# Optimization experiments

Measured on AMD Instinct MI355X. Metric: run time of the kernel, lower is better.

## Reference

```python
import jax, jax.numpy as jnp
import numpy as np

N = 20000; E = 320000; IN = 512; H = 4; C = 128; HC = H * C; SD = 2; SE = 128
NEG = 0.01      # nn.LeakyReLU default slope (post-norm activations)
ATT_NEG = 0.2   # GATv2 attention LeakyReLU slope


def _gatv2(x, wl, bl, wr, br, att, bias, src, dst, concat):
    # PyG GATv2Conv (eval mode, add_self_loops already applied to src/dst)
    n = x.shape[0]
    xl = (x @ wl.T + bl).reshape(n, H, C)   # source-side projection
    xr = (x @ wr.T + br).reshape(n, H, C)   # target-side projection
    e = jax.nn.leaky_relu(xl[src] + xr[dst], ATT_NEG)        # [Etot, H, C]
    logits = jnp.einsum('ehc,hc->eh', e, att)                # [Etot, H]
    m = jax.ops.segment_max(logits, dst, num_segments=n)     # segment softmax over dst
    ez = jnp.exp(logits - m[dst])
    denom = jax.ops.segment_sum(ez, dst, num_segments=n)
    alpha = ez / denom[dst]
    out = jax.ops.segment_sum(xl[src] * alpha[:, :, None], dst, num_segments=n)  # [n, H, C]
    out = out.reshape(n, HC) if concat else out.mean(axis=1)
    return out + bias, alpha


def _bn(x, g, b):
    # BatchNorm1d, training-mode batch statistics (biased variance), eps=1e-5
    mu = x.mean(0)
    v = x.var(0)
    return g * (x - mu) * jax.lax.rsqrt(v + 1e-5) + b


def setup_inputs() -> dict:
    key = jax.random.key(0)
    ks = jax.random.split(key, 20)
    p = lambda i, shape: jax.random.normal(ks[i], shape, jnp.float32) * 0.05
    return dict(
        x=jax.random.normal(ks[0], (N, IN), jnp.float32),
        edge_index=jax.random.randint(ks[1], (2, E), 0, N),
        spatial_coords=jax.random.uniform(ks[2], (N, SD), dtype=jnp.float32),
        w1_l=p(3, (HC, IN)), b1_l=jnp.zeros((HC,)), w1_r=p(4, (HC, IN)), b1_r=jnp.zeros((HC,)),
        att1=p(5, (H, C)), bias1=jnp.zeros((HC,)), bn1_g=jnp.ones((HC,)), bn1_b=jnp.zeros((HC,)),
        w2_l=p(6, (HC, HC)), b2_l=jnp.zeros((HC,)), w2_r=p(7, (HC, HC)), b2_r=jnp.zeros((HC,)),
        att2=p(8, (H, C)), bias2=jnp.zeros((HC,)), bn2_g=jnp.ones((HC,)), bn2_b=jnp.zeros((HC,)),
        w3_l=p(9, (HC, HC)), b3_l=jnp.zeros((HC,)), w3_r=p(10, (HC, HC)), b3_r=jnp.zeros((HC,)),
        att3=p(11, (H, C)), bias3=jnp.zeros((C,)), bn3_g=jnp.ones((C,)), bn3_b=jnp.zeros((C,)),
        sp_w1=p(12, (SE, SD)), sp_b1=jnp.zeros((SE,)),
        sp_w2=p(13, (C, SE)), sp_b2=jnp.zeros((C,)),
        mha_in_w=p(14, (3 * SE, SE)), mha_in_b=jnp.zeros((3 * SE,)),
        mha_out_w=p(15, (SE, SE)), mha_out_b=jnp.zeros((SE,)),
        gate_w=p(16, (1, 2 * C)), gate_b=jnp.zeros((1,)),
    )


def reference(x, edge_index, spatial_coords,
              w1_l, b1_l, w1_r, b1_r, att1, bias1, bn1_g, bn1_b,
              w2_l, b2_l, w2_r, b2_r, att2, bias2, bn2_g, bn2_b,
              w3_l, b3_l, w3_r, b3_r, att3, bias3, bn3_g, bn3_b,
              sp_w1, sp_b1, sp_w2, sp_b2,
              mha_in_w, mha_in_b, mha_out_w, mha_out_b,
              gate_w, gate_b):
    loop = jnp.arange(N)
    src = jnp.concatenate([edge_index[0], loop])  # add self loops (PyG default)
    dst = jnp.concatenate([edge_index[1], loop])

    h1, a1 = _gatv2(x, w1_l, b1_l, w1_r, b1_r, att1, bias1, src, dst, True)
    h1 = jax.nn.leaky_relu(_bn(h1, bn1_g, bn1_b), NEG)
    h2, a2 = _gatv2(h1, w2_l, b2_l, w2_r, b2_r, att2, bias2, src, dst, True)
    h2 = jax.nn.leaky_relu(_bn(h2, bn2_g, bn2_b), NEG)
    z, a3 = _gatv2(h2, w3_l, b3_l, w3_r, b3_r, att3, bias3, src, dst, False)
    z = jax.nn.leaky_relu(_bn(z, bn3_g, bn3_b), NEG)

    # spatial embedding MLP (Linear -> LeakyReLU -> Linear -> LeakyReLU)
    emb = jax.nn.leaky_relu(spatial_coords @ sp_w1.T + sp_b1, NEG)
    emb = jax.nn.leaky_relu(emb @ sp_w2.T + sp_b2, NEG)
    # MultiheadAttention over a length-1 sequence: softmax over a single key is 1,
    # so output = W_o (W_v e + b_v) + b_o
    wv = mha_in_w[2 * SE:]
    bv = mha_in_b[2 * SE:]
    sp = (emb @ wv.T + bv) @ mha_out_w.T + mha_out_b  # [N, C]

    gate = jax.nn.softmax(jnp.concatenate([z, sp], axis=-1) @ gate_w.T + gate_b, axis=-1)  # [N,1] (all ones: size-1 softmax, faithful to source)
    z = gate * z + (1.0 - gate) * sp
    return z, a1, a2, a3, gate
```

## Files before the change

kernel.cpp:

```cpp
#include <hip/hip_runtime.h>
#include <math.h>

#define NN 20000
#define EE 320000
#define ETOT 340000
#define DEGCAP 128

typedef __attribute__((ext_vector_type(8))) short short8;
typedef __attribute__((ext_vector_type(4))) float f32x4;

__device__ __forceinline__ float lrelu(float x, float s) { return fmaxf(x, s * x); }
__device__ __forceinline__ float bf2f(ushort u) {
    union { uint i; float f; } c;
    c.i = ((uint)u) << 16;
    return c.f;
}
__device__ __forceinline__ ushort f2bf(float f) {
    uint u = __float_as_uint(f);
    uint r = (u + 0x7FFFu + ((u >> 16) & 1u)) >> 16;
    return (ushort)r;
}
__device__ __forceinline__ void gload16(const ushort* g, const ushort* l) {
    __builtin_amdgcn_global_load_lds((const __attribute__((address_space(1))) void*)g,
                                     (__attribute__((address_space(3))) void*)l, 16, 0, 0);
}

__global__ __launch_bounds__(1024) void k_scan(const int* __restrict__ counts, int* __restrict__ rstart) {
    __shared__ int sm[1024];
    int t = threadIdx.x;
    const int CH = 20;
    int base = t * CH;
    int loc[CH];
    int s = 0;
#pragma unroll
    for (int j = 0; j < CH; ++j) {
        int idx = base + j;
        int v = (idx < NN) ? counts[idx] : 0;
        loc[j] = s;
        s += v;
    }
    sm[t] = s;
    __syncthreads();
    for (int o = 1; o < 1024; o <<= 1) {
        int v = (t >= o) ? sm[t - o] : 0;
        __syncthreads();
        if (t >= o) sm[t] += v;
        __syncthreads();
    }
    int off = sm[t] - s;
#pragma unroll
    for (int j = 0; j < CH; ++j) {
        int idx = base + j;
        if (idx < NN) rstart[idx] = off + loc[j];
    }
    if (t == 1023) rstart[NN] = sm[1023];
}

__global__ void k_scatter(const int* __restrict__ ei, const int* __restrict__ rstart,
                          int* __restrict__ cursor, int* __restrict__ csr) {
    int i = blockIdx.x * blockDim.x + threadIdx.x;
    if (i >= ETOT) return;
    int d = (i < EE) ? ei[EE + i] : (i - EE);
    int pos = atomicAdd(&cursor[d], 1);
    csr[rstart[d] + pos] = i;
}

__global__ void k_prep(const float* __restrict__ x, const float* __restrict__ w0, const float* __restrict__ w1,
                       const float* __restrict__ w2, const float* __restrict__ w3, const float* __restrict__ w4,
                       const float* __restrict__ w5, ushort* __restrict__ xout, ushort* __restrict__ wout,
                       const int* __restrict__ ei, int* __restrict__ counts) {
    int b = blockIdx.x, t = threadIdx.x;
    if (b < 10000) {
        int i = (b * 256 + t) * 4;
        float4 v = *(const float4*)(x + i);
        uint2 pk;
        pk.x = (uint)f2bf(v.x) | ((uint)f2bf(v.y) << 16);
        pk.y = (uint)f2bf(v.z) | ((uint)f2bf(v.w) << 16);
        *(uint2*)(xout + i) = pk;
    } else if (b < 11536) {
        int q = (b - 10000) * 256 + t;
        if (q >= 6 * 65536) return;
        int which = q >> 16;
        int off = (q & 65535) << 2;
        const float* src = which == 0 ? w0 : which == 1 ? w1 : which == 2 ? w2 : which == 3 ? w3 : which == 4 ? w4 : w5;
        float4 v = *(const float4*)(src + off);
        uint2 pk;
        pk.x = (uint)f2bf(v.x) | ((uint)f2bf(v.y) << 16);
        pk.y = (uint)f2bf(v.z) | ((uint)f2bf(v.w) << 16);
        *(uint2*)(wout + which * 262144 + off) = pk;
    } else {
        int i = (b - 11536) * 256 + t;
        if (i >= ETOT) return;
        int d = (i < EE) ? ei[EE + i] : (i - EE);
        atomicAdd(&counts[d], 1);
    }
}

__global__ __launch_bounds__(512, 4) void k_gemm2(const ushort* __restrict__ A, const ushort* __restrict__ W,
                                                  const float* __restrict__ bl, const float* __restrict__ br,
                                                  ushort* __restrict__ XL, ushort* __restrict__ XR) {
    __shared__ ushort As[4][128][8];
    __shared__ ushort Bs[4][128][8];
    int tid = threadIdx.x;
    int wid = tid >> 6, lane = tid & 63;
    int wm = wid >> 2, wn = wid & 3;
    int bid = blockIdx.x;
    int L = (bid & 7) * 157 + (bid >> 3);
    int mt = L >> 3, nt = L & 7;
    int bm = mt * 128, bn = nt * 128;
    const float* bias = (nt >= 4) ? br : bl;
    ushort* C = (nt >= 4) ? XR : XL;
    int cb = bn - ((nt >= 4) ? 512 : 0);
    int lrow = lane & 15, lslot = lane >> 4;
    int r = tid & 127, ks = tid >> 7;
    int ar = bm + r;
    if (ar >= NN) ar = NN - 1;
    const ushort* gA = A + (size_t)ar * 512 + ks * 8;
    const ushort* gB = W + (size_t)(bn + r) * 512 + ks * 8;
    const ushort* lA = &As[0][0][0] + (size_t)(wid * 64) * 8;
    const ushort* lB = &Bs[0][0][0] + (size_t)(wid * 64) * 8;
    f32x4 acc[4][2] = {};
    for (int k0 = 0; k0 < 512; k0 += 32) {
        gload16(gA + k0, lA);
        gload16(gB + k0, lB);
        __syncthreads();
        short8 af[4], bfr[2];
#pragma unroll
        for (int i = 0; i < 4; ++i) af[i] = *(const short8*)&As[lslot][wm * 64 + i * 16 + lrow][0];
#pragma unroll
        for (int j = 0; j < 2; ++j) bfr[j] = *(const short8*)&Bs[lslot][wn * 32 + j * 16 + lrow][0];
#pragma unroll
        for (int i = 0; i < 4; ++i)
#pragma unroll
            for (int j = 0; j < 2; ++j)
                acc[i][j] = __builtin_amdgcn_mfma_f32_16x16x32_bf16(af[i], bfr[j], acc[i][j], 0, 0, 0);
        __syncthreads();
    }
#pragma unroll
    for (int i = 0; i < 4; ++i) {
#pragma unroll
        for (int j = 0; j < 2; ++j) {
            int gcol = cb + wn * 32 + j * 16 + lrow;
            float bv = bias[gcol];
            int growb = bm + wm * 64 + i * 16 + lslot * 4;
#pragma unroll
            for (int reg = 0; reg < 4; ++reg) {
                int grow = growb + reg;
                if (grow < NN) C[(size_t)grow * 512 + gcol] = f2bf(acc[i][j][reg] + bv);
            }
        }
    }
}

__global__ __launch_bounds__(256) void k_fused(const ushort* __restrict__ xl, const ushort* __restrict__ xr,
                                               const float* __restrict__ att, const int* __restrict__ ei,
                                               const int* __restrict__ rstart, const int* __restrict__ csr,
                                               const float* __restrict__ bias, float* __restrict__ alpha,
                                               ushort* __restrict__ dest, float* __restrict__ bzero, int meanHeads) {
    __shared__ float slg[4][DEGCAP][4];
    __shared__ int ssrc[4][DEGCAP];
    if (blockIdx.x == 0) {
        float4 z = {0.f, 0.f, 0.f, 0.f};
        ((float4*)bzero)[threadIdx.x] = z;
    }
    int w = threadIdx.x >> 6, lane = threadIdx.x & 63;
    int node = blockIdx.x * 4 + w;
    int s0 = rstart[node];
    int deg = rstart[node + 1] - s0;
    int hh = lane >> 4;
    short8 xrv = *(const short8*)(xr + (size_t)node * 512 + lane * 8);
    const float4* at = (const float4*)att + lane * 2;
    float4 a0 = at[0], a1 = at[1];
    float attv[8] = {a0.x, a0.y, a0.z, a0.w, a1.x, a1.y, a1.z, a1.w};
    float xrf[8];
#pragma unroll
    for (int j = 0; j < 8; ++j) xrf[j] = bf2f((ushort)xrv[j]);
    for (int i = lane; i < deg; i += 64) {
        int e = csr[s0 + i];
        ssrc[w][i < DEGCAP ? i : 0] = (e < EE) ? ei[e] : e - EE;
    }
    float m = -1e30f, denom = 0.f;
    float acc[8] = {};
    int scur = ssrc[w][0];
    short8 row = *(const short8*)(xl + (size_t)scur * 512 + lane * 8);
    for (int i = 0; i < deg; ++i) {
        short8 rown = row;
        if (i + 1 < deg) {
            int sn = ssrc[w][(i + 1) < DEGCAP ? (i + 1) : 0];
            rown = *(const short8*)(xl + (size_t)sn * 512 + lane * 8);
        }
        float rf[8];
#pragma unroll
        for (int j = 0; j < 8; ++j) rf[j] = bf2f((ushort)row[j]);
        float p = 0.f;
#pragma unroll
        for (int j = 0; j < 8; ++j) {
            float e = rf[j] + xrf[j];
            p = fmaf(fmaxf(e, 0.2f * e), attv[j], p);
        }
        p += __shfl_xor(p, 1);
        p += __shfl_xor(p, 2);
        p += __shfl_xor(p, 4);
        p += __shfl_xor(p, 8);
        if ((lane & 15) == 0 && i < DEGCAP) slg[w][i][hh] = p;
        if (p <= m) {
            float wg = __expf(p - m);
            denom += wg;
#pragma unroll
            for (int j = 0; j < 8; ++j) acc[j] = fmaf(wg, rf[j], acc[j]);
        } else {
            float sc = __expf(m - p);
            denom = fmaf(denom, sc, 1.f);
#pragma unroll
            for (int j = 0; j < 8; ++j) acc[j] = fmaf(acc[j], sc, rf[j]);
            m = p;
        }
        row = rown;
    }
    float rd = 1.f / denom;
    float m0 = __shfl(m, 0), m1 = __shfl(m, 16), m2 = __shfl(m, 32), m3 = __shfl(m, 48);
    float r0 = __shfl(rd, 0), r1 = __shfl(rd, 16), r2 = __shfl(rd, 32), r3 = __shfl(rd, 48);
    int nal = deg < DEGCAP ? deg : DEGCAP;
    for (int i = lane; i < nal; i += 64) {
        int e = csr[s0 + i];
        float4 l = *(const float4*)&slg[w][i][0];
        float4 av;
        av.x = __expf(l.x - m0) * r0;
        av.y = __expf(l.y - m1) * r1;
        av.z = __expf(l.z - m2) * r2;
        av.w = __expf(l.w - m3) * r3;
        *(float4*)(alpha + (size_t)e * 4) = av;
    }
#pragma unroll
    for (int j = 0; j < 8; ++j) acc[j] *= rd;
    if (!meanHeads) {
        int c = lane * 8;
        short8 o;
#pragma unroll
        for (int j = 0; j < 8; ++j) o[j] = (short)f2bf(acc[j] + bias[c + j]);
        *(short8*)(dest + (size_t)node * 512 + c) = o;
    } else {
#pragma unroll
        for (int j = 0; j < 8; ++j) {
            acc[j] += __shfl_xor(acc[j], 16);
            acc[j] += __shfl_xor(acc[j], 32);
        }
        if (lane < 16) {
            int c = lane * 8;
            short8 o;
#pragma unroll
            for (int j = 0; j < 8; ++j) o[j] = (short)f2bf(0.25f * acc[j] + bias[c + j]);
            *(short8*)(dest + (size_t)node * 128 + c) = o;
        }
    }
}

__global__ void k_bnstats(const ushort* __restrict__ X, float* __restrict__ s, float* __restrict__ s2, int npairs) {
    int t = threadIdx.x;
    if (t >= npairs) return;
    float a0 = 0.f, a1 = 0.f, q0 = 0.f, q1 = 0.f;
    for (int r = blockIdx.x; r < NN; r += gridDim.x) {
        uint p = ((const uint*)X)[r * npairs + t];
        float v0 = bf2f((ushort)(p & 0xffffu));
        float v1 = bf2f((ushort)(p >> 16));
        a0 += v0; q0 += v0 * v0;
        a1 += v1; q1 += v1 * v1;
    }
    atomicAdd(&s[2 * t], a0);
    atomicAdd(&s[2 * t + 1], a1);
    atomicAdd(&s2[2 * t], q0);
    atomicAdd(&s2[2 * t + 1], q1);
}

__global__ void k_bnapply(const ushort* __restrict__ X, const float* __restrict__ g, const float* __restrict__ b,
                          const float* __restrict__ bsum, const float* __restrict__ bsq, float* __restrict__ Yf,
                          ushort* __restrict__ Yb, float* __restrict__ gout, int mask4, int n4) {
    int i = blockIdx.x * blockDim.x + threadIdx.x;
    if (gout && i < NN) gout[i] = 1.0f;
    if (i >= n4) return;
    int c = (i & mask4) << 2;
    uint2 p = ((const uint2*)X)[i];
    float x0 = bf2f((ushort)(p.x & 0xffffu)), x1 = bf2f((ushort)(p.x >> 16));
    float x2 = bf2f((ushort)(p.y & 0xffffu)), x3 = bf2f((ushort)(p.y >> 16));
    float4 S = *(const float4*)(bsum + c);
    float4 Q = *(const float4*)(bsq + c);
    float4 G = *(const float4*)(g + c);
    float4 B = *(const float4*)(b + c);
    const float inv = 1.f / NN;
    float mx = S.x * inv, my = S.y * inv, mz = S.z * inv, mw = S.w * inv;
    float rx = rsqrtf(Q.x * inv - mx * mx + 1e-5f);
    float ry = rsqrtf(Q.y * inv - my * my + 1e-5f);
    float rz = rsqrtf(Q.z * inv - mz * mz + 1e-5f);
    float rw = rsqrtf(Q.w * inv - mw * mw + 1e-5f);
    float4 y;
    y.x = lrelu(G.x * (x0 - mx) * rx + B.x, 0.01f);
    y.y = lrelu(G.y * (x1 - my) * ry + B.y, 0.01f);
    y.z = lrelu(G.z * (x2 - mz) * rz + B.z, 0.01f);
    y.w = lrelu(G.w * (x3 - mw) * rw + B.w, 0.01f);
    if (Yb) {
        uint2 pk;
        pk.x = (uint)f2bf(y.x) | ((uint)f2bf(y.y) << 16);
        pk.y = (uint)f2bf(y.z) | ((uint)f2bf(y.w) << 16);
        *(uint2*)(Yb + (size_t)i * 4) = pk;
    } else {
        ((float4*)Yf)[i] = y;
    }
}

extern "C" void kernel_launch(void* const* d_in, const int* in_sizes, int n_in,
                              void* d_out, int out_size, void* d_ws, size_t ws_size,
                              hipStream_t stream) {
    const float* x = (const float*)d_in[0];
    const int* ei = (const int*)d_in[1];
    const float* wl[3] = {(const float*)d_in[3], (const float*)d_in[11], (const float*)d_in[19]};
    const float* bl[3] = {(const float*)d_in[4], (const float*)d_in[12], (const float*)d_in[20]};
    const float* wr[3] = {(const float*)d_in[5], (const float*)d_in[13], (const float*)d_in[21]};
    const float* br[3] = {(const float*)d_in[6], (const float*)d_in[14], (const float*)d_in[22]};
    const float* att[3] = {(const float*)d_in[7], (const float*)d_in[15], (const float*)d_in[23]};
    const float* bias[3] = {(const float*)d_in[8], (const float*)d_in[16], (const float*)d_in[24]};
    const float* bng[3] = {(const float*)d_in[9], (const float*)d_in[17], (const float*)d_in[25]};
    const float* bnb[3] = {(const float*)d_in[10], (const float*)d_in[18], (const float*)d_in[26]};

    ushort* a_bf = (ushort*)d_ws;
    ushort* xl_bf = a_bf + (size_t)NN * 512;
    ushort* xr_bf = xl_bf + (size_t)NN * 512;
    ushort* h_bf = xr_bf + (size_t)NN * 512;
    ushort* wbuf = h_bf + (size_t)NN * 512;
    float* fp = (float*)(wbuf + 6 * 262144);
    float* bsum = fp;
    float* bsq = bsum + 512;
    int* counts = (int*)(bsq + 512);
    int* cursor = counts + NN;
    int* rstart = cursor + NN;
    int* csr = rstart + (NN + 1);
    size_t need = (size_t)((char*)(csr + ETOT) - (char*)d_ws);
    if (ws_size < need) return;

    float* out = (float*)d_out;
    float* zout = out;
    float* aout[3] = {out + 2560000, out + 3920000, out + 5280000};
    float* gout = out + 6640000;

    hipMemsetAsync(counts, 0, 2 * NN * sizeof(int), stream);
    k_prep<<<12865, 256, 0, stream>>>(x, wl[0], wr[0], wl[1], wr[1], wl[2], wr[2], a_bf, wbuf, ei, counts);
    k_scan<<<1, 1024, 0, stream>>>(counts, rstart);
    k_scatter<<<(ETOT + 255) / 256, 256, 0, stream>>>(ei, rstart, cursor, csr);

    for (int l = 0; l < 3; ++l) {
        const ushort* wb = wbuf + (size_t)l * 524288;
        k_gemm2<<<1256, 512, 0, stream>>>(a_bf, wb, bl[l], br[l], xl_bf, xr_bf);
        int ncols = (l == 2) ? 128 : 512;
        k_fused<<<NN / 4, 256, 0, stream>>>(xl_bf, xr_bf, att[l], ei, rstart, csr, bias[l], aout[l], h_bf,
                                            bsum, (l == 2) ? 1 : 0);
        k_bnstats<<<240, 256, 0, stream>>>(h_bf, bsum, bsq, ncols / 2);
        int n4 = NN * ncols / 4;
        if (l < 2) {
            k_bnapply<<<(n4 + 255) / 256, 256, 0, stream>>>(h_bf, bng[l], bnb[l], bsum, bsq, nullptr, a_bf,
                                                            nullptr, ncols / 4 - 1, n4);
        } else {
            k_bnapply<<<(n4 + 255) / 256, 256, 0, stream>>>(h_bf, bng[l], bnb[l], bsum, bsq, zout, nullptr,
                                                            gout, ncols / 4 - 1, n4);
        }
    }
}
```

Baseline: 655.1 us.

## Double-buffer GEMM LDS loads and fuse BN stats/apply with grid barrier

The GEMM k-loop now double-buffers its LDS tiles: the next K slice is issued with async global-to-LDS loads before the current one is computed, and explicit vmcnt waits and raw barriers replace __syncthreads. BatchNorm statistics and the normalize/activation pass are merged into one persistent 240-block kernel. It uses an atomic arrival counter as a grid-wide barrier, which removes one launch per layer and keeps the data in cache for the second pass. The grid barrier assumes all 240 blocks are co-resident, and the vmcnt accounting must match the number of outstanding loads.

```diff
diff --git a/kernel.cpp b/kernel.cpp
--- a/kernel.cpp
+++ b/kernel.cpp
@@ -99,8 +99,8 @@
 __global__ __launch_bounds__(512, 4) void k_gemm2(const ushort* __restrict__ A, const ushort* __restrict__ W,
                                                   const float* __restrict__ bl, const float* __restrict__ br,
                                                   ushort* __restrict__ XL, ushort* __restrict__ XR) {
-    __shared__ ushort As[4][128][8];
-    __shared__ ushort Bs[4][128][8];
+    __shared__ ushort As[2][4][128][8];
+    __shared__ ushort Bs[2][4][128][8];
     int tid = threadIdx.x;
     int wid = tid >> 6, lane = tid & 63;
     int wm = wid >> 2, wn = wid & 3;
@@ -117,24 +117,34 @@
     if (ar >= NN) ar = NN - 1;
     const ushort* gA = A + (size_t)ar * 512 + ks * 8;
     const ushort* gB = W + (size_t)(bn + r) * 512 + ks * 8;
-    const ushort* lA = &As[0][0][0] + (size_t)(wid * 64) * 8;
-    const ushort* lB = &Bs[0][0][0] + (size_t)(wid * 64) * 8;
+    const ushort* lA[2] = {&As[0][0][0][0] + (size_t)(wid * 64) * 8, &As[1][0][0][0] + (size_t)(wid * 64) * 8};
+    const ushort* lB[2] = {&Bs[0][0][0][0] + (size_t)(wid * 64) * 8, &Bs[1][0][0][0] + (size_t)(wid * 64) * 8};
     f32x4 acc[4][2] = {};
-    for (int k0 = 0; k0 < 512; k0 += 32) {
-        gload16(gA + k0, lA);
-        gload16(gB + k0, lB);
-        __syncthreads();
+    gload16(gA, lA[0]);
+    gload16(gB, lB[0]);
+#pragma unroll
+    for (int t = 0; t < 16; ++t) {
+        const int cur = t & 1;
+        if (t < 15) {
+            int k0 = (t + 1) * 32;
+            gload16(gA + k0, lA[cur ^ 1]);
+            gload16(gB + k0, lB[cur ^ 1]);
+            asm volatile("s_waitcnt vmcnt(2)" ::: "memory");
+        } else {
+            asm volatile("s_waitcnt vmcnt(0)" ::: "memory");
+        }
+        __builtin_amdgcn_s_barrier();
         short8 af[4], bfr[2];
 #pragma unroll
-        for (int i = 0; i < 4; ++i) af[i] = *(const short8*)&As[lslot][wm * 64 + i * 16 + lrow][0];
-#pragma unroll
-        for (int j = 0; j < 2; ++j) bfr[j] = *(const short8*)&Bs[lslot][wn * 32 + j * 16 + lrow][0];
+        for (int i = 0; i < 4; ++i) af[i] = *(const short8*)&As[cur][lslot][wm * 64 + i * 16 + lrow][0];
+#pragma unroll
+        for (int j = 0; j < 2; ++j) bfr[j] = *(const short8*)&Bs[cur][lslot][wn * 32 + j * 16 + lrow][0];
 #pragma unroll
         for (int i = 0; i < 4; ++i)
 #pragma unroll
             for (int j = 0; j < 2; ++j)
                 acc[i][j] = __builtin_amdgcn_mfma_f32_16x16x32_bf16(af[i], bfr[j], acc[i][j], 0, 0, 0);
-        __syncthreads();
+        __builtin_amdgcn_s_barrier();
     }
 #pragma unroll
     for (int i = 0; i < 4; ++i) {
@@ -255,55 +265,76 @@
     }
 }
 
-__global__ void k_bnstats(const ushort* __restrict__ X, float* __restrict__ s, float* __restrict__ s2, int npairs) {
+__global__ __launch_bounds__(256) void k_bn(const ushort* __restrict__ X, const float* __restrict__ g,
+                                            const float* __restrict__ b, float* __restrict__ bsum,
+                                            float* __restrict__ bsq, float* __restrict__ Yf,
+                                            ushort* __restrict__ Yb, float* __restrict__ gout,
+                                            int* __restrict__ arrive, int ncols) {
     int t = threadIdx.x;
-    if (t >= npairs) return;
-    float a0 = 0.f, a1 = 0.f, q0 = 0.f, q1 = 0.f;
-    for (int r = blockIdx.x; r < NN; r += gridDim.x) {
-        uint p = ((const uint*)X)[r * npairs + t];
-        float v0 = bf2f((ushort)(p & 0xffffu));
-        float v1 = bf2f((ushort)(p >> 16));
-        a0 += v0; q0 += v0 * v0;
-        a1 += v1; q1 += v1 * v1;
-    }
-    atomicAdd(&s[2 * t], a0);
-    atomicAdd(&s[2 * t + 1], a1);
-    atomicAdd(&s2[2 * t], q0);
-    atomicAdd(&s2[2 * t + 1], q1);
-}
-
-__global__ void k_bnapply(const ushort* __restrict__ X, const float* __restrict__ g, const float* __restrict__ b,
-                          const float* __restrict__ bsum, const float* __restrict__ bsq, float* __restrict__ Yf,
-                          ushort* __restrict__ Yb, float* __restrict__ gout, int mask4, int n4) {
-    int i = blockIdx.x * blockDim.x + threadIdx.x;
-    if (gout && i < NN) gout[i] = 1.0f;
-    if (i >= n4) return;
-    int c = (i & mask4) << 2;
-    uint2 p = ((const uint2*)X)[i];
-    float x0 = bf2f((ushort)(p.x & 0xffffu)), x1 = bf2f((ushort)(p.x >> 16));
-    float x2 = bf2f((ushort)(p.y & 0xffffu)), x3 = bf2f((ushort)(p.y >> 16));
-    float4 S = *(const float4*)(bsum + c);
-    float4 Q = *(const float4*)(bsq + c);
+    int npairs = ncols >> 1;
+    if (t < npairs) {
+        float a0 = 0.f, a1 = 0.f, q0 = 0.f, q1 = 0.f;
+        for (int r = blockIdx.x; r < NN; r += gridDim.x) {
+            uint p = ((const uint*)X)[r * npairs + t];
+            float v0 = bf2f((ushort)(p & 0xffffu));
+            float v1 = bf2f((ushort)(p >> 16));
+            a0 += v0; q0 += v0 * v0;
+            a1 += v1; q1 += v1 * v1;
+        }
+        atomicAdd(&bsum[2 * t], a0);
+        atomicAdd(&bsum[2 * t + 1], a1);
+        atomicAdd(&bsq[2 * t], q0);
+        atomicAdd(&bsq[2 * t + 1], q1);
+    }
+    __syncthreads();
+    if (t == 0) {
+        atomicAdd(arrive, 1);
+        while (__hip_atomic_load(arrive, __ATOMIC_ACQUIRE, __HIP_MEMORY_SCOPE_AGENT) < (int)gridDim.x)
+            __builtin_amdgcn_s_sleep(16);
+    }
+    __syncthreads();
+    int q4 = ncols >> 2;
+    int gtid = blockIdx.x * 256 + t;
+    int qc = gtid & (q4 - 1);
+    int c = qc << 2;
+    int rstep = (gridDim.x * 256) / q4;
+    const float inv = 1.f / NN;
+    float S0 = __hip_atomic_load(&bsum[c + 0], __ATOMIC_RELAXED, __HIP_MEMORY_SCOPE_AGENT);
+    float S1 = __hip_atomic_load(&bsum[c + 1], __ATOMIC_RELAXED, __HIP_MEMORY_SCOPE_AGENT);
+    float S2 = __hip_atomic_load(&bsum[c + 2], __ATOMIC_RELAXED, __HIP_MEMORY_SCOPE_AGENT);
+    float S3 = __hip_atomic_load(&bsum[c + 3], __ATOMIC_RELAXED, __HIP_MEMORY_SCOPE_AGENT);
+    float Q0 = __hip_atomic_load(&bsq[c + 0], __ATOMIC_RELAXED, __HIP_MEMORY_SCOPE_AGENT);
+    float Q1 = __hip_atomic_load(&bsq[c + 1], __ATOMIC_RELAXED, __HIP_MEMORY_SCOPE_AGENT);
+    float Q2 = __hip_atomic_load(&bsq[c + 2], __ATOMIC_RELAXED, __HIP_MEMORY_SCOPE_AGENT);
+    float Q3 = __hip_atomic_load(&bsq[c + 3], __ATOMIC_RELAXED, __HIP_MEMORY_SCOPE_AGENT);
+    float mx = S0 * inv, my = S1 * inv, mz = S2 * inv, mw = S3 * inv;
+    float rx = rsqrtf(Q0 * inv - mx * mx + 1e-5f);
+    float ry = rsqrtf(Q1 * inv - my * my + 1e-5f);
+    float rz = rsqrtf(Q2 * inv - mz * mz + 1e-5f);
+    float rw = rsqrtf(Q3 * inv - mw * mw + 1e-5f);
     float4 G = *(const float4*)(g + c);
     float4 B = *(const float4*)(b + c);
-    const float inv = 1.f / NN;
-    float mx = S.x * inv, my = S.y * inv, mz = S.z * inv, mw = S.w * inv;
-    float rx = rsqrtf(Q.x * inv - mx * mx + 1e-5f);
-    float ry = rsqrtf(Q.y * inv - my * my + 1e-5f);
-    float rz = rsqrtf(Q.z * inv - mz * mz + 1e-5f);
-    float rw = rsqrtf(Q.w * inv - mw * mw + 1e-5f);
-    float4 y;
-    y.x = lrelu(G.x * (x0 - mx) * rx + B.x, 0.01f);
-    y.y = lrelu(G.y * (x1 - my) * ry + B.y, 0.01f);
-    y.z = lrelu(G.z * (x2 - mz) * rz + B.z, 0.01f);
-    y.w = lrelu(G.w * (x3 - mw) * rw + B.w, 0.01f);
-    if (Yb) {
-        uint2 pk;
-        pk.x = (uint)f2bf(y.x) | ((uint)f2bf(y.y) << 16);
-        pk.y = (uint)f2bf(y.z) | ((uint)f2bf(y.w) << 16);
-        *(uint2*)(Yb + (size_t)i * 4) = pk;
-    } else {
-        ((float4*)Yf)[i] = y;
+    for (int row = gtid / q4; row < NN; row += rstep) {
+        int i = row * q4 + qc;
+        uint2 p = ((const uint2*)X)[i];
+        float x0 = bf2f((ushort)(p.x & 0xffffu)), x1 = bf2f((ushort)(p.x >> 16));
+        float x2 = bf2f((ushort)(p.y & 0xffffu)), x3 = bf2f((ushort)(p.y >> 16));
+        float4 y;
+        y.x = lrelu(G.x * (x0 - mx) * rx + B.x, 0.01f);
+        y.y = lrelu(G.y * (x1 - my) * ry + B.y, 0.01f);
+        y.z = lrelu(G.z * (x2 - mz) * rz + B.z, 0.01f);
+        y.w = lrelu(G.w * (x3 - mw) * rw + B.w, 0.01f);
+        if (Yb) {
+            uint2 pk;
+            pk.x = (uint)f2bf(y.x) | ((uint)f2bf(y.y) << 16);
+            pk.y = (uint)f2bf(y.z) | ((uint)f2bf(y.w) << 16);
+            *(uint2*)(Yb + (size_t)i * 4) = pk;
+        } else {
+            ((float4*)Yf)[i] = y;
+        }
+    }
+    if (gout) {
+        for (int i = gtid; i < NN; i += gridDim.x * 256) gout[i] = 1.0f;
     }
 }
 
@@ -331,7 +362,8 @@
     float* bsq = bsum + 512;
     int* counts = (int*)(bsq + 512);
     int* cursor = counts + NN;
-    int* rstart = cursor + NN;
+    int* arrive = cursor + NN;
+    int* rstart = arrive + 4;
     int* csr = rstart + (NN + 1);
     size_t need = (size_t)((char*)(csr + ETOT) - (char*)d_ws);
     if (ws_size < need) return;
@@ -341,7 +373,7 @@
     float* aout[3] = {out + 2560000, out + 3920000, out + 5280000};
     float* gout = out + 6640000;
 
-    hipMemsetAsync(counts, 0, 2 * NN * sizeof(int), stream);
+    hipMemsetAsync(counts, 0, (2 * NN + 4) * sizeof(int), stream);
     k_prep<<<12865, 256, 0, stream>>>(x, wl[0], wr[0], wl[1], wr[1], wl[2], wr[2], a_bf, wbuf, ei, counts);
     k_scan<<<1, 1024, 0, stream>>>(counts, rstart);
     k_scatter<<<(ETOT + 255) / 256, 256, 0, stream>>>(ei, rstart, cursor, csr);
@@ -352,14 +384,12 @@
         int ncols = (l == 2) ? 128 : 512;
         k_fused<<<NN / 4, 256, 0, stream>>>(xl_bf, xr_bf, att[l], ei, rstart, csr, bias[l], aout[l], h_bf,
                                             bsum, (l == 2) ? 1 : 0);
-        k_bnstats<<<240, 256, 0, stream>>>(h_bf, bsum, bsq, ncols / 2);
-        int n4 = NN * ncols / 4;
         if (l < 2) {
-            k_bnapply<<<(n4 + 255) / 256, 256, 0, stream>>>(h_bf, bng[l], bnb[l], bsum, bsq, nullptr, a_bf,
-                                                            nullptr, ncols / 4 - 1, n4);
+            k_bn<<<240, 256, 0, stream>>>(h_bf, bng[l], bnb[l], bsum, bsq, nullptr, a_bf, nullptr,
+                                          arrive + l, ncols);
         } else {
-            k_bnapply<<<(n4 + 255) / 256, 256, 0, stream>>>(h_bf, bng[l], bnb[l], bsum, bsq, zout, nullptr,
-                                                            gout, ncols / 4 - 1, n4);
-        }
-    }
-}
+            k_bn<<<240, 256, 0, stream>>>(h_bf, bng[l], bnb[l], bsum, bsq, zout, nullptr, gout,
+                                          arrive + l, ncols);
+        }
+    }
+}
```

Measured after the change: 690.9 us. 5.5% more time.

## Fuse BN statistics into attention kernel and double-buffer GEMM LDS loads

Applied to the files above, without the earlier changes.

Removes the separate batch-norm statistics kernel by accumulating per-column sum and sum-of-squares in shared memory inside the fused attention kernel and flushing them to global with atomics. Zeroing of the stats buffer moves into the GEMM kernel. The GEMM also gets double-buffered LDS with async global-to-LDS loads and explicit waitcnt/barriers, so the next K-tile loads while the current one computes. In exchange, the fused kernel issues many shared atomics and more global atomics, and the stats are taken in fp32 before bf16 rounding.

```diff
diff --git a/kernel.cpp b/kernel.cpp
--- a/kernel.cpp
+++ b/kernel.cpp
@@ -98,13 +98,18 @@
 
 __global__ __launch_bounds__(512, 4) void k_gemm2(const ushort* __restrict__ A, const ushort* __restrict__ W,
                                                   const float* __restrict__ bl, const float* __restrict__ br,
-                                                  ushort* __restrict__ XL, ushort* __restrict__ XR) {
-    __shared__ ushort As[4][128][8];
-    __shared__ ushort Bs[4][128][8];
+                                                  ushort* __restrict__ XL, ushort* __restrict__ XR,
+                                                  float* __restrict__ bz) {
+    __shared__ ushort As[2][4][128][8];
+    __shared__ ushort Bs[2][4][128][8];
     int tid = threadIdx.x;
     int wid = tid >> 6, lane = tid & 63;
     int wm = wid >> 2, wn = wid & 3;
     int bid = blockIdx.x;
+    if (bid == 0) {
+        float2 z = {0.f, 0.f};
+        ((float2*)bz)[tid] = z;
+    }
     int L = (bid & 7) * 157 + (bid >> 3);
     int mt = L >> 3, nt = L & 7;
     int bm = mt * 128, bn = nt * 128;
@@ -117,24 +122,34 @@
     if (ar >= NN) ar = NN - 1;
     const ushort* gA = A + (size_t)ar * 512 + ks * 8;
     const ushort* gB = W + (size_t)(bn + r) * 512 + ks * 8;
-    const ushort* lA = &As[0][0][0] + (size_t)(wid * 64) * 8;
-    const ushort* lB = &Bs[0][0][0] + (size_t)(wid * 64) * 8;
+    const ushort* lA[2] = {&As[0][0][0][0] + (size_t)(wid * 64) * 8, &As[1][0][0][0] + (size_t)(wid * 64) * 8};
+    const ushort* lB[2] = {&Bs[0][0][0][0] + (size_t)(wid * 64) * 8, &Bs[1][0][0][0] + (size_t)(wid * 64) * 8};
     f32x4 acc[4][2] = {};
-    for (int k0 = 0; k0 < 512; k0 += 32) {
-        gload16(gA + k0, lA);
-        gload16(gB + k0, lB);
-        __syncthreads();
+    gload16(gA, lA[0]);
+    gload16(gB, lB[0]);
+#pragma unroll
+    for (int t = 0; t < 16; ++t) {
+        const int cur = t & 1;
+        if (t < 15) {
+            int k0 = (t + 1) * 32;
+            gload16(gA + k0, lA[cur ^ 1]);
+            gload16(gB + k0, lB[cur ^ 1]);
+            asm volatile("s_waitcnt vmcnt(2)" ::: "memory");
+        } else {
+            asm volatile("s_waitcnt vmcnt(0)" ::: "memory");
+        }
+        __builtin_amdgcn_s_barrier();
         short8 af[4], bfr[2];
 #pragma unroll
-        for (int i = 0; i < 4; ++i) af[i] = *(const short8*)&As[lslot][wm * 64 + i * 16 + lrow][0];
-#pragma unroll
-        for (int j = 0; j < 2; ++j) bfr[j] = *(const short8*)&Bs[lslot][wn * 32 + j * 16 + lrow][0];
+        for (int i = 0; i < 4; ++i) af[i] = *(const short8*)&As[cur][lslot][wm * 64 + i * 16 + lrow][0];
+#pragma unroll
+        for (int j = 0; j < 2; ++j) bfr[j] = *(const short8*)&Bs[cur][lslot][wn * 32 + j * 16 + lrow][0];
 #pragma unroll
         for (int i = 0; i < 4; ++i)
 #pragma unroll
             for (int j = 0; j < 2; ++j)
                 acc[i][j] = __builtin_amdgcn_mfma_f32_16x16x32_bf16(af[i], bfr[j], acc[i][j], 0, 0, 0);
-        __syncthreads();
+        __builtin_amdgcn_s_barrier();
     }
 #pragma unroll
     for (int i = 0; i < 4; ++i) {
@@ -156,13 +171,14 @@
                                                const float* __restrict__ att, const int* __restrict__ ei,
                                                const int* __restrict__ rstart, const int* __restrict__ csr,
                                                const float* __restrict__ bias, float* __restrict__ alpha,
-                                               ushort* __restrict__ dest, float* __restrict__ bzero, int meanHeads) {
+                                               ushort* __restrict__ dest, float* __restrict__ bstat,
+                                               int meanHeads) {
     __shared__ float slg[4][DEGCAP][4];
     __shared__ int ssrc[4][DEGCAP];
-    if (blockIdx.x == 0) {
-        float4 z = {0.f, 0.f, 0.f, 0.f};
-        ((float4*)bzero)[threadIdx.x] = z;
-    }
+    __shared__ float sstat[1024];
+#pragma unroll
+    for (int i = 0; i < 4; ++i) sstat[threadIdx.x + i * 256] = 0.f;
+    __syncthreads();
     int w = threadIdx.x >> 6, lane = threadIdx.x & 63;
     int node = blockIdx.x * 4 + w;
     int s0 = rstart[node];
@@ -237,7 +253,12 @@
         int c = lane * 8;
         short8 o;
 #pragma unroll
-        for (int j = 0; j < 8; ++j) o[j] = (short)f2bf(acc[j] + bias[c + j]);
+        for (int j = 0; j < 8; ++j) {
+            float y = acc[j] + bias[c + j];
+            o[j] = (short)f2bf(y);
+            atomicAdd(&sstat[c + j], y);
+            atomicAdd(&sstat[512 + c + j], y * y);
+        }
         *(short8*)(dest + (size_t)node * 512 + c) = o;
     } else {
 #pragma unroll
@@ -249,27 +270,22 @@
             int c = lane * 8;
             short8 o;
 #pragma unroll
-            for (int j = 0; j < 8; ++j) o[j] = (short)f2bf(0.25f * acc[j] + bias[c + j]);
+            for (int j = 0; j < 8; ++j) {
+                float y = 0.25f * acc[j] + bias[c + j];
+                o[j] = (short)f2bf(y);
+                atomicAdd(&sstat[c + j], y);
+                atomicAdd(&sstat[512 + c + j], y * y);
+            }
             *(short8*)(dest + (size_t)node * 128 + c) = o;
         }
     }
-}
-
-__global__ void k_bnstats(const ushort* __restrict__ X, float* __restrict__ s, float* __restrict__ s2, int npairs) {
-    int t = threadIdx.x;
-    if (t >= npairs) return;
-    float a0 = 0.f, a1 = 0.f, q0 = 0.f, q1 = 0.f;
-    for (int r = blockIdx.x; r < NN; r += gridDim.x) {
-        uint p = ((const uint*)X)[r * npairs + t];
-        float v0 = bf2f((ushort)(p & 0xffffu));
-        float v1 = bf2f((ushort)(p >> 16));
-        a0 += v0; q0 += v0 * v0;
-        a1 += v1; q1 += v1 * v1;
-    }
-    atomicAdd(&s[2 * t], a0);
-    atomicAdd(&s[2 * t + 1], a1);
-    atomicAdd(&s2[2 * t], q0);
-    atomicAdd(&s2[2 * t + 1], q1);
+    __syncthreads();
+#pragma unroll
+    for (int i = 0; i < 4; ++i) {
+        int idx = threadIdx.x + i * 256;
+        float v = sstat[idx];
+        if (v != 0.f) atomicAdd(&bstat[idx], v);
+    }
 }
 
 __global__ void k_bnapply(const ushort* __restrict__ X, const float* __restrict__ g, const float* __restrict__ b,
@@ -348,11 +364,10 @@
 
     for (int l = 0; l < 3; ++l) {
         const ushort* wb = wbuf + (size_t)l * 524288;
-        k_gemm2<<<1256, 512, 0, stream>>>(a_bf, wb, bl[l], br[l], xl_bf, xr_bf);
+        k_gemm2<<<1256, 512, 0, stream>>>(a_bf, wb, bl[l], br[l], xl_bf, xr_bf, bsum);
         int ncols = (l == 2) ? 128 : 512;
         k_fused<<<NN / 4, 256, 0, stream>>>(xl_bf, xr_bf, att[l], ei, rstart, csr, bias[l], aout[l], h_bf,
                                             bsum, (l == 2) ? 1 : 0);
-        k_bnstats<<<240, 256, 0, stream>>>(h_bf, bsum, bsq, ncols / 2);
         int n4 = NN * ncols / 4;
         if (l < 2) {
             k_bnapply<<<(n4 + 255) / 256, 256, 0, stream>>>(h_bf, bng[l], bnb[l], bsum, bsq, nullptr, a_bf,
```

Result: slower. 866.8 us (+32.3%).
